# Kernel tuning notes

Hardware: AMD Instinct MI355X
Metric: run time of the kernel (lower is better)

Reference implementation:

```python
import jax, jax.numpy as jnp
import numpy as np

B, S, H = 4, 2048, 1024
NH = 16
DH = H // NH  # 64


def setup_inputs() -> dict:
    key = jax.random.key(0)
    ks = jax.random.split(key, 11)
    s = 1.0 / np.sqrt(H)
    inp = {
        "key": jax.random.normal(ks[0], (B, S, H), jnp.float32),
        "value": jax.random.normal(ks[1], (B, S, H), jnp.float32),
        "query": jax.random.normal(ks[2], (B, S, H), jnp.float32),
        # linear_layers[0] -> applied to query, [1] -> key, [2] -> value
        "wq": jax.random.normal(ks[3], (H, H), jnp.float32) * s,
        "bq": jnp.zeros((H,), jnp.float32),
        "wk": jax.random.normal(ks[4], (H, H), jnp.float32) * s,
        "bk": jnp.zeros((H,), jnp.float32),
        "wv": jax.random.normal(ks[5], (H, H), jnp.float32) * s,
        "bv": jnp.zeros((H,), jnp.float32),
        "wo": jax.random.normal(ks[6], (H, H), jnp.float32) * s,
        "bo": jnp.zeros((H,), jnp.float32),
    }
    return inp


def reference(key, value, query, wq, bq, wk, bk, wv, bv, wo, bo):
    # QKV projections; split heads -> [B, NH, S, DH]
    def proj(x, w, b):
        y = jnp.einsum("bsh,hd->bsd", x, w) + b
        return y.reshape(B, S, NH, DH).transpose(0, 2, 1, 3)

    q = proj(query, wq, bq)
    k = proj(key, wk, bk)
    v = proj(value, wv, bv)

    scores = jnp.einsum("bnqd,bnkd->bnqk", q, k) / jnp.sqrt(jnp.float32(DH))
    probs = jax.nn.softmax(scores, axis=-1)  # dropout p=0 -> identity
    out = jnp.einsum("bnqk,bnkd->bnqd", probs, v)
    out = out.transpose(0, 2, 1, 3).reshape(B, S, H)
    return jnp.einsum("bsh,hd->bsd", out, wo) + bo
```

## Files before the change

### kernel.cpp

```cpp
#include <hip/hip_runtime.h>
#include <hip/hip_bf16.h>

constexpr int kB = 4, kS = 2048, kH = 1024, kNH = 16, kDH = 64;
constexpr int kM = kB * kS;

typedef short short8 __attribute__((ext_vector_type(8)));
typedef float f32x4 __attribute__((ext_vector_type(4)));
typedef float f32x16 __attribute__((ext_vector_type(16)));

__device__ inline unsigned int pack2bf16(float lo, float hi) {
  __hip_bfloat162 h;
  h.x = __float2bfloat16(lo);
  h.y = __float2bfloat16(hi);
  unsigned int u;
  __builtin_memcpy(&u, &h, 4);
  return u;
}

__device__ inline void gload_lds16(const unsigned short* g, unsigned short* l) {
  auto* gp = (const __attribute__((address_space(1))) unsigned int*)(uintptr_t)g;
  auto* lp = (__attribute__((address_space(3))) unsigned int*)(unsigned int)(uintptr_t)l;
  __builtin_amdgcn_global_load_lds(gp, lp, 16, 0, 0);
}

__global__ __launch_bounds__(256) void f32_to_bf16_vec3(
    const float* __restrict__ i0, const float* __restrict__ i1,
    const float* __restrict__ i2, __hip_bfloat16* __restrict__ o0,
    __hip_bfloat16* __restrict__ o1, __hip_bfloat16* __restrict__ o2) {
  const int z = blockIdx.y;
  const float* in = z == 0 ? i0 : z == 1 ? i1 : i2;
  __hip_bfloat16* out = z == 0 ? o0 : z == 1 ? o1 : o2;
  const int i = blockIdx.x * 256 + threadIdx.x;
  const float4 v = ((const float4*)in)[i];
  union { __hip_bfloat16 h[4]; uint2 u; } p;
  p.h[0] = __float2bfloat16(v.x);
  p.h[1] = __float2bfloat16(v.y);
  p.h[2] = __float2bfloat16(v.z);
  p.h[3] = __float2bfloat16(v.w);
  ((uint2*)out)[i] = p.u;
}

__global__ __launch_bounds__(256) void transpose4_f32_to_bf16(
    const float* __restrict__ w0, const float* __restrict__ w1,
    const float* __restrict__ w2, const float* __restrict__ w3,
    __hip_bfloat16* __restrict__ o0, __hip_bfloat16* __restrict__ o1,
    __hip_bfloat16* __restrict__ o2, __hip_bfloat16* __restrict__ o3) {
  const int z = blockIdx.z;
  const float* in = z == 0 ? w0 : z == 1 ? w1 : z == 2 ? w2 : w3;
  __hip_bfloat16* out = z == 0 ? o0 : z == 1 ? o1 : z == 2 ? o2 : o3;
  constexpr int R = kH, C = kH;
  __shared__ float t[32][33];
  const int r0 = blockIdx.y * 32, c0 = blockIdx.x * 32;
  const int tx = threadIdx.x, ty = threadIdx.y;
#pragma unroll
  for (int i = 0; i < 32; i += 8)
    t[ty + i][tx] = in[(size_t)(r0 + ty + i) * C + c0 + tx];
  __syncthreads();
#pragma unroll
  for (int i = 0; i < 32; i += 8)
    out[(size_t)(c0 + ty + i) * R + r0 + tx] = __float2bfloat16(t[tx][ty + i]);
}

__global__ __launch_bounds__(256, 4) void gemm_qkv(
    const unsigned short* __restrict__ A0, const unsigned short* __restrict__ A1,
    const unsigned short* __restrict__ A2, const unsigned short* __restrict__ W0,
    const unsigned short* __restrict__ W1, const unsigned short* __restrict__ W2,
    const float* __restrict__ b0, const float* __restrict__ b1,
    const float* __restrict__ b2, unsigned short* __restrict__ O0,
    unsigned short* __restrict__ O1, unsigned short* __restrict__ O2) {
  constexpr int K = kH;
  __shared__ unsigned short sA[2][128 * 32];
  __shared__ unsigned short sB[2][128 * 32];
  const int tid = threadIdx.x;
  const int wave = tid >> 6, lane = tid & 63;
  const int n16 = lane & 15, quad = lane >> 4;

  const int hw = blockIdx.x + (blockIdx.y << 3) + ((int)blockIdx.z << 9);
  const int wid = (hw & 7) * 192 + (hw >> 3);
  const int z = wid >> 9;
  const int rem = wid & 511;
  const int n0 = (rem & 7) * 128, m0 = (rem >> 3) * 128;

  const unsigned short* A = z == 0 ? A0 : z == 1 ? A1 : A2;
  const unsigned short* W = z == 0 ? W0 : z == 1 ? W1 : W2;
  const float* bias = z == 0 ? b0 : z == 1 ? b1 : b2;

  const int rh = (wave >> 1) * 64, ch = (wave & 1) * 64;
  const int srow = 32 * wave + (lane >> 2);
  const int sk = (lane & 3) * 8;
  const unsigned short* gA = A + (size_t)(m0 + srow) * K + sk;
  const unsigned short* gB = W + (size_t)(n0 + srow) * K + sk;

  const f32x4 zero4 = {0.f, 0.f, 0.f, 0.f};
  f32x4 acc[4][4];
#pragma unroll
  for (int i = 0; i < 4; ++i)
#pragma unroll
    for (int j = 0; j < 4; ++j) acc[i][j] = zero4;

#pragma unroll
  for (int j = 0; j < 2; ++j) {
    gload_lds16(gA + (size_t)(16 * j) * K, &sA[0][(32 * wave + 16 * j) * 32]);
    gload_lds16(gB + (size_t)(16 * j) * K, &sB[0][(32 * wave + 16 * j) * 32]);
  }
  __syncthreads();

  int cur = 0;
  for (int k0 = 0; k0 < K; k0 += 32) {
    const int kn = (k0 + 32 < K) ? k0 + 32 : 0;
#pragma unroll
    for (int j = 0; j < 2; ++j) {
      gload_lds16(gA + (size_t)(16 * j) * K + kn,
                  &sA[cur ^ 1][(32 * wave + 16 * j) * 32]);
      gload_lds16(gB + (size_t)(16 * j) * K + kn,
                  &sB[cur ^ 1][(32 * wave + 16 * j) * 32]);
    }

    short8 af[4], bfr[4];
#pragma unroll
    for (int i = 0; i < 4; ++i)
      af[i] = *(const short8*)&sA[cur][(rh + i * 16 + n16) * 32 + quad * 8];
#pragma unroll
    for (int i = 0; i < 4; ++i)
      bfr[i] = *(const short8*)&sB[cur][(ch + i * 16 + n16) * 32 + quad * 8];
#pragma unroll
    for (int mi = 0; mi < 4; ++mi)
#pragma unroll
      for (int ni = 0; ni < 4; ++ni)
        acc[mi][ni] = __builtin_amdgcn_mfma_f32_16x16x32_bf16(
            af[mi], bfr[ni], acc[mi][ni], 0, 0, 0);

    __syncthreads();
    cur ^= 1;
  }

  __hip_bfloat16* Obf = (__hip_bfloat16*)(z == 0 ? O0 : z == 1 ? O1 : O2);
  const float osc = z == 0 ? 0.18033688011112042f : 1.0f;
#pragma unroll
  for (int ni = 0; ni < 4; ++ni) {
    const int n = n0 + ch + ni * 16 + n16;
    const float bv = bias[n];
    const int hh = n >> 6, dd = n & 63;
#pragma unroll
    for (int mi = 0; mi < 4; ++mi) {
      const int mbase = m0 + rh + mi * 16 + quad * 4;
      const int bb = mbase >> 11, ss = mbase & 2047;
      if (z == 2) {
        const size_t idx = ((size_t)(bb * kNH + hh) * kDH + dd) * kS + ss;
        uint2 w;
        w.x = pack2bf16(acc[mi][ni][0] + bv, acc[mi][ni][1] + bv);
        w.y = pack2bf16(acc[mi][ni][2] + bv, acc[mi][ni][3] + bv);
        *(uint2*)&Obf[idx] = w;
      } else {
        const size_t base = ((size_t)(bb * kNH + hh) * kS + ss) * kDH + dd;
#pragma unroll
        for (int r = 0; r < 4; ++r)
          Obf[base + (size_t)r * kDH] =
              __float2bfloat16((acc[mi][ni][r] + bv) * osc);
      }
    }
  }
}

__global__ __launch_bounds__(256) void gemm_out(
    const unsigned short* __restrict__ A, const unsigned short* __restrict__ Bt,
    const float* __restrict__ bias, float* __restrict__ C, int M, int N, int K) {
  __shared__ unsigned short sA[2][128 * 32];
  __shared__ unsigned short sB[2][128 * 32];
  const int tid = threadIdx.x;
  const int wave = tid >> 6, lane = tid & 63;
  const int n16 = lane & 15, quad = lane >> 4;

  const int hw = blockIdx.x + blockIdx.y * gridDim.x;
  const int cpx = (gridDim.x * gridDim.y) >> 3;
  const int wid = (hw & 7) * cpx + (hw >> 3);
  const int n0 = (wid % gridDim.x) * 128, m0 = (wid / gridDim.x) * 128;

  const int rh = (wave >> 1) * 64, ch = (wave & 1) * 64;
  const int srow = 32 * wave + (lane >> 2);
  const int sk = (lane & 3) * 8;
  const unsigned short* gA = A + (size_t)(m0 + srow) * K + sk;
  const unsigned short* gB = Bt + (size_t)(n0 + srow) * K + sk;

  const f32x4 zero4 = {0.f, 0.f, 0.f, 0.f};
  f32x4 acc[4][4];
#pragma unroll
  for (int i = 0; i < 4; ++i)
#pragma unroll
    for (int j = 0; j < 4; ++j) acc[i][j] = zero4;

#pragma unroll
  for (int j = 0; j < 2; ++j) {
    gload_lds16(gA + (size_t)(16 * j) * K, &sA[0][(32 * wave + 16 * j) * 32]);
    gload_lds16(gB + (size_t)(16 * j) * K, &sB[0][(32 * wave + 16 * j) * 32]);
  }
  __syncthreads();

  int cur = 0;
  for (int k0 = 0; k0 < K; k0 += 32) {
    const int kn = (k0 + 32 < K) ? k0 + 32 : 0;
#pragma unroll
    for (int j = 0; j < 2; ++j) {
      gload_lds16(gA + (size_t)(16 * j) * K + kn,
                  &sA[cur ^ 1][(32 * wave + 16 * j) * 32]);
      gload_lds16(gB + (size_t)(16 * j) * K + kn,
                  &sB[cur ^ 1][(32 * wave + 16 * j) * 32]);
    }

    short8 af[4], bfr[4];
#pragma unroll
    for (int i = 0; i < 4; ++i)
      af[i] = *(const short8*)&sA[cur][(rh + i * 16 + n16) * 32 + quad * 8];
#pragma unroll
    for (int i = 0; i < 4; ++i)
      bfr[i] = *(const short8*)&sB[cur][(ch + i * 16 + n16) * 32 + quad * 8];
#pragma unroll
    for (int mi = 0; mi < 4; ++mi)
#pragma unroll
      for (int ni = 0; ni < 4; ++ni)
        acc[mi][ni] = __builtin_amdgcn_mfma_f32_16x16x32_bf16(
            af[mi], bfr[ni], acc[mi][ni], 0, 0, 0);

    __syncthreads();
    cur ^= 1;
  }

#pragma unroll
  for (int ni = 0; ni < 4; ++ni) {
    const int n = n0 + ch + ni * 16 + n16;
    const float bv = bias[n];
#pragma unroll
    for (int mi = 0; mi < 4; ++mi) {
#pragma unroll
      for (int r = 0; r < 4; ++r) {
        const int m = m0 + rh + mi * 16 + quad * 4 + r;
        C[(size_t)m * N + n] = acc[mi][ni][r] + bv;
      }
    }
  }
}

__global__ __launch_bounds__(256, 2) void attn_mfma(
    const unsigned short* __restrict__ Q, const unsigned short* __restrict__ K,
    const unsigned short* __restrict__ V, __hip_bfloat16* __restrict__ ctx) {
  __shared__ unsigned short sK[64][72];
  __shared__ unsigned short sVT[64][72];

  const int tid = threadIdx.x;
  const int wave = tid >> 6, lane = tid & 63;
  const int l31 = lane & 31, hi = lane >> 5;

  const int hw = blockIdx.x + ((int)blockIdx.y << 3);
  const int wid = (hw & 7) * 64 + (hw >> 3);
  const int bh = wid >> 3;
  const int q0 = (wid & 7) * 256;

  const unsigned short* Qb = Q + (size_t)bh * (kS * kDH);
  const unsigned short* Kb = K + (size_t)bh * (kS * kDH);
  const unsigned short* Vb = V + (size_t)bh * (kS * kDH);

  const int qbase = q0 + wave * 64;
  short8 qf[2][4];
#pragma unroll
  for (int g = 0; g < 2; ++g)
#pragma unroll
    for (int c = 0; c < 4; ++c)
      qf[g][c] = *(const short8*)(Qb + (size_t)(qbase + g * 32 + l31) * kDH +
                                  c * 16 + hi * 8);

  float l_part0 = 0.f, l_part1 = 0.f;
  f32x16 oacc[2][2];
#pragma unroll
  for (int g = 0; g < 2; ++g)
#pragma unroll
    for (int db = 0; db < 2; ++db)
#pragma unroll
      for (int i = 0; i < 16; ++i) oacc[g][db][i] = 0.f;

  const int srow = tid >> 2, scol = (tid & 3) * 16;

  uint4 ka, kb2, va, vb;
  auto loadtile = [&](int kk) {
    ka = *(const uint4*)(Kb + (size_t)(kk + srow) * kDH + scol);
    kb2 = *(const uint4*)(Kb + (size_t)(kk + srow) * kDH + scol + 8);
    va = *(const uint4*)(Vb + (size_t)srow * kS + kk + scol);
    vb = *(const uint4*)(Vb + (size_t)srow * kS + kk + scol + 8);
  };
  auto writetile = [&]() {
    *(uint4*)&sK[srow][scol] = ka;
    *(uint4*)&sK[srow][scol + 8] = kb2;
    *(uint4*)&sVT[srow][scol] = va;
    *(uint4*)&sVT[srow][scol + 8] = vb;
  };

  loadtile(0);
  writetile();
  __syncthreads();

  for (int k0 = 0; k0 < kS; k0 += 64) {
    const int kn = (k0 + 64 < kS) ? k0 + 64 : 0;
    loadtile(kn);

    short8 pfrag[2][4];
#pragma unroll
    for (int kbi = 0; kbi < 2; ++kbi) {
      short8 af[4];
#pragma unroll
      for (int c = 0; c < 4; ++c)
        af[c] = *(const short8*)&sK[kbi * 32 + l31][c * 16 + hi * 8];
#pragma unroll
      for (int g = 0; g < 2; ++g) {
        f32x16 sacc;
#pragma unroll
        for (int i = 0; i < 16; ++i) sacc[i] = 0.f;
        __builtin_amdgcn_s_setprio(1);
#pragma unroll
        for (int c = 0; c < 4; ++c)
          sacc = __builtin_amdgcn_mfma_f32_32x32x16_bf16(af[c], qf[g][c],
                                                         sacc, 0, 0, 0);
        __builtin_amdgcn_s_setprio(0);

        unsigned int w[8];
        float lp = 0.f;
#pragma unroll
        for (int m = 0; m < 8; ++m) {
          const float p0 = __builtin_amdgcn_exp2f(sacc[2 * m]);
          const float p1 = __builtin_amdgcn_exp2f(sacc[2 * m + 1]);
          lp += p0 + p1;
          w[m] = pack2bf16(p0, p1);
        }
        if (g == 0) l_part0 += lp; else l_part1 += lp;
        asm("v_permlane32_swap_b32 %0, %1" : "+v"(w[0]), "+v"(w[2]));
        asm("v_permlane32_swap_b32 %0, %1" : "+v"(w[1]), "+v"(w[3]));
        asm("v_permlane32_swap_b32 %0, %1" : "+v"(w[4]), "+v"(w[6]));
        asm("v_permlane32_swap_b32 %0, %1" : "+v"(w[5]), "+v"(w[7]));
        union { unsigned int u[4]; short8 s; } f0, f1;
        f0.u[0] = w[0]; f0.u[1] = w[1]; f0.u[2] = w[2]; f0.u[3] = w[3];
        f1.u[0] = w[4]; f1.u[1] = w[5]; f1.u[2] = w[6]; f1.u[3] = w[7];
        pfrag[g][kbi * 2] = f0.s;
        pfrag[g][kbi * 2 + 1] = f1.s;
      }
    }

    __builtin_amdgcn_s_setprio(1);
#pragma unroll
    for (int t = 0; t < 4; ++t) {
#pragma unroll
      for (int db = 0; db < 2; ++db) {
        const short8 vf = *(const short8*)&sVT[db * 32 + l31][t * 16 + hi * 8];
        oacc[0][db] = __builtin_amdgcn_mfma_f32_32x32x16_bf16(vf, pfrag[0][t],
                                                              oacc[0][db], 0, 0, 0);
        oacc[1][db] = __builtin_amdgcn_mfma_f32_32x32x16_bf16(vf, pfrag[1][t],
                                                              oacc[1][db], 0, 0, 0);
      }
    }
    __builtin_amdgcn_s_setprio(0);

    __syncthreads();
    writetile();
    __syncthreads();
  }

  const float l0 = l_part0 + __shfl_xor(l_part0, 32);
  const float l1 = l_part1 + __shfl_xor(l_part1, 32);
  const float inv[2] = {1.f / l0, 1.f / l1};

  const int bb = bh >> 4, hh = bh & 15;
#pragma unroll
  for (int g = 0; g < 2; ++g) {
    const int qrow = qbase + g * 32 + l31;
    __hip_bfloat16* dst = ctx + ((size_t)(bb * kS + qrow)) * kH + hh * kDH;
#pragma unroll
    for (int db = 0; db < 2; ++db) {
#pragma unroll
      for (int gr = 0; gr < 4; ++gr) {
        uint2 w;
        w.x = pack2bf16(oacc[g][db][4 * gr] * inv[g],
                        oacc[g][db][4 * gr + 1] * inv[g]);
        w.y = pack2bf16(oacc[g][db][4 * gr + 2] * inv[g],
                        oacc[g][db][4 * gr + 3] * inv[g]);
        *(uint2*)(dst + db * 32 + gr * 8 + hi * 4) = w;
      }
    }
  }
}

extern "C" void kernel_launch(void* const* d_in, const int* in_sizes, int n_in,
                              void* d_out, int out_size, void* d_ws, size_t ws_size,
                              hipStream_t stream) {
  const float* key   = (const float*)d_in[0];
  const float* value = (const float*)d_in[1];
  const float* query = (const float*)d_in[2];
  const float* wq = (const float*)d_in[3];
  const float* bq = (const float*)d_in[4];
  const float* wk = (const float*)d_in[5];
  const float* bk = (const float*)d_in[6];
  const float* wv = (const float*)d_in[7];
  const float* bv = (const float*)d_in[8];
  const float* wo = (const float*)d_in[9];
  const float* bo = (const float*)d_in[10];
  float* out = (float*)d_out;

  const size_t SZ = (size_t)kB * kS * kH;
  unsigned short* p = (unsigned short*)d_ws;
  unsigned short* actb = p; p += SZ;
  unsigned short* Qh   = p; p += SZ;
  unsigned short* Kh   = p; p += SZ;
  unsigned short* Vh   = p; p += SZ;
  unsigned short* ctxh = p; p += SZ;
  unsigned short* wqt  = p; p += (size_t)kH * kH;
  unsigned short* wkt  = p; p += (size_t)kH * kH;
  unsigned short* wvt  = p; p += (size_t)kH * kH;
  unsigned short* wot  = p; p += (size_t)kH * kH;
  unsigned short* actk = ctxh;
  unsigned short* actv = (unsigned short*)out;

  const dim3 tb(32, 8);
  const dim3 tg(kH / 32, kH / 32, 4);
  transpose4_f32_to_bf16<<<tg, tb, 0, stream>>>(
      wq, wk, wv, wo, (__hip_bfloat16*)wqt, (__hip_bfloat16*)wkt,
      (__hip_bfloat16*)wvt, (__hip_bfloat16*)wot);

  const int cvblocks = (int)(SZ / 4 / 256);
  f32_to_bf16_vec3<<<dim3(cvblocks, 3), 256, 0, stream>>>(
      query, key, value, (__hip_bfloat16*)actb, (__hip_bfloat16*)actk,
      (__hip_bfloat16*)actv);

  gemm_qkv<<<dim3(kH / 128, kM / 128, 3), 256, 0, stream>>>(
      actb, actk, actv, wqt, wkt, wvt, bq, bk, bv, Qh, Kh, Vh);

  dim3 ga(kS / 256, kB * kNH);
  attn_mfma<<<ga, 256, 0, stream>>>(Qh, Kh, Vh, (__hip_bfloat16*)ctxh);

  dim3 gg(kH / 128, kM / 128);
  gemm_out<<<gg, 256, 0, stream>>>(ctxh, wot, bo, out, kM, kH, kH);
}
```

Measured before the change: 338.0 us.

## Triple-buffer GEMM K-loop and double-buffer attention K/V tiles

Replaces the double-buffered GEMM K-loop in both projection kernels with a shared triple-buffered macro. It prefetches two tiles ahead, uses explicit vmcnt waits with a single barrier per iteration, and raises MFMA priority. The attention kernel gets double-buffered K/V LDS tiles, which removes one of its two barriers per iteration. The extra LDS use lowers the GEMM occupancy hint from 4 to 3 blocks.

After: 336.3 us. Within noise of the previous version (-0.5%).

```diff
diff --git a/kernel.cpp b/kernel.cpp
--- a/kernel.cpp
+++ b/kernel.cpp
@@ -61,7 +61,53 @@
     out[(size_t)(c0 + ty + i) * R + r0 + tx] = __float2bfloat16(t[tx][ty + i]);
 }
 
-__global__ __launch_bounds__(256, 4) void gemm_qkv(
+#define GEMM_KLOOP(sA, sB, gA, gB, K, acc)                                    \
+  {                                                                           \
+    const int NIT = (K) / 32;                                                 \
+    _Pragma("unroll") for (int j = 0; j < 2; ++j) {                           \
+      gload_lds16(gA + (size_t)(16 * j) * (K), &sA[0][(32 * wave + 16 * j) * 32]); \
+      gload_lds16(gB + (size_t)(16 * j) * (K), &sB[0][(32 * wave + 16 * j) * 32]); \
+    }                                                                         \
+    _Pragma("unroll") for (int j = 0; j < 2; ++j) {                           \
+      gload_lds16(gA + (size_t)(16 * j) * (K) + 32, &sA[1][(32 * wave + 16 * j) * 32]); \
+      gload_lds16(gB + (size_t)(16 * j) * (K) + 32, &sB[1][(32 * wave + 16 * j) * 32]); \
+    }                                                                         \
+    asm volatile("s_waitcnt vmcnt(4) lgkmcnt(0)" ::: "memory");               \
+    __builtin_amdgcn_s_barrier();                                             \
+    __builtin_amdgcn_sched_barrier(0);                                        \
+    for (int t = 0; t < NIT; ++t) {                                           \
+      const int cur = t % 3;                                                  \
+      short8 af[4], bfr[4];                                                   \
+      _Pragma("unroll") for (int i = 0; i < 4; ++i)                           \
+          af[i] = *(const short8*)&sA[cur][(rh + i * 16 + n16) * 32 + quad * 8]; \
+      _Pragma("unroll") for (int i = 0; i < 4; ++i)                           \
+          bfr[i] = *(const short8*)&sB[cur][(ch + i * 16 + n16) * 32 + quad * 8]; \
+      if (t + 2 < NIT) {                                                      \
+        const int nxt = (t + 2) % 3;                                          \
+        const int kk = (t + 2) * 32;                                          \
+        _Pragma("unroll") for (int j = 0; j < 2; ++j) {                       \
+          gload_lds16(gA + (size_t)(16 * j) * (K) + kk,                       \
+                      &sA[nxt][(32 * wave + 16 * j) * 32]);                   \
+          gload_lds16(gB + (size_t)(16 * j) * (K) + kk,                       \
+                      &sB[nxt][(32 * wave + 16 * j) * 32]);                   \
+        }                                                                     \
+      }                                                                       \
+      __builtin_amdgcn_s_setprio(1);                                          \
+      _Pragma("unroll") for (int mi = 0; mi < 4; ++mi)                        \
+          _Pragma("unroll") for (int ni = 0; ni < 4; ++ni)                    \
+              acc[mi][ni] = __builtin_amdgcn_mfma_f32_16x16x32_bf16(          \
+                  af[mi], bfr[ni], acc[mi][ni], 0, 0, 0);                     \
+      __builtin_amdgcn_s_setprio(0);                                          \
+      if (t + 2 < NIT)                                                        \
+        asm volatile("s_waitcnt vmcnt(4) lgkmcnt(0)" ::: "memory");           \
+      else                                                                    \
+        asm volatile("s_waitcnt vmcnt(0) lgkmcnt(0)" ::: "memory");           \
+      __builtin_amdgcn_s_barrier();                                           \
+      __builtin_amdgcn_sched_barrier(0);                                      \
+    }                                                                         \
+  }
+
+__global__ __launch_bounds__(256, 3) void gemm_qkv(
     const unsigned short* __restrict__ A0, const unsigned short* __restrict__ A1,
     const unsigned short* __restrict__ A2, const unsigned short* __restrict__ W0,
     const unsigned short* __restrict__ W1, const unsigned short* __restrict__ W2,
@@ -69,8 +115,8 @@
     const float* __restrict__ b2, unsigned short* __restrict__ O0,
     unsigned short* __restrict__ O1, unsigned short* __restrict__ O2) {
   constexpr int K = kH;
-  __shared__ unsigned short sA[2][128 * 32];
-  __shared__ unsigned short sB[2][128 * 32];
+  __shared__ unsigned short sA[3][128 * 32];
+  __shared__ unsigned short sB[3][128 * 32];
   const int tid = threadIdx.x;
   const int wave = tid >> 6, lane = tid & 63;
   const int n16 = lane & 15, quad = lane >> 4;
@@ -98,41 +144,7 @@
 #pragma unroll
     for (int j = 0; j < 4; ++j) acc[i][j] = zero4;
 
-#pragma unroll
-  for (int j = 0; j < 2; ++j) {
-    gload_lds16(gA + (size_t)(16 * j) * K, &sA[0][(32 * wave + 16 * j) * 32]);
-    gload_lds16(gB + (size_t)(16 * j) * K, &sB[0][(32 * wave + 16 * j) * 32]);
-  }
-  __syncthreads();
-
-  int cur = 0;
-  for (int k0 = 0; k0 < K; k0 += 32) {
-    const int kn = (k0 + 32 < K) ? k0 + 32 : 0;
-#pragma unroll
-    for (int j = 0; j < 2; ++j) {
-      gload_lds16(gA + (size_t)(16 * j) * K + kn,
-                  &sA[cur ^ 1][(32 * wave + 16 * j) * 32]);
-      gload_lds16(gB + (size_t)(16 * j) * K + kn,
-                  &sB[cur ^ 1][(32 * wave + 16 * j) * 32]);
-    }
-
-    short8 af[4], bfr[4];
-#pragma unroll
-    for (int i = 0; i < 4; ++i)
-      af[i] = *(const short8*)&sA[cur][(rh + i * 16 + n16) * 32 + quad * 8];
-#pragma unroll
-    for (int i = 0; i < 4; ++i)
-      bfr[i] = *(const short8*)&sB[cur][(ch + i * 16 + n16) * 32 + quad * 8];
-#pragma unroll
-    for (int mi = 0; mi < 4; ++mi)
-#pragma unroll
-      for (int ni = 0; ni < 4; ++ni)
-        acc[mi][ni] = __builtin_amdgcn_mfma_f32_16x16x32_bf16(
-            af[mi], bfr[ni], acc[mi][ni], 0, 0, 0);
-
-    __syncthreads();
-    cur ^= 1;
-  }
+  GEMM_KLOOP(sA, sB, gA, gB, K, acc)
 
   __hip_bfloat16* Obf = (__hip_bfloat16*)(z == 0 ? O0 : z == 1 ? O1 : O2);
   const float osc = z == 0 ? 0.18033688011112042f : 1.0f;
@@ -162,11 +174,11 @@
   }
 }
 
-__global__ __launch_bounds__(256) void gemm_out(
+__global__ __launch_bounds__(256, 3) void gemm_out(
     const unsigned short* __restrict__ A, const unsigned short* __restrict__ Bt,
     const float* __restrict__ bias, float* __restrict__ C, int M, int N, int K) {
-  __shared__ unsigned short sA[2][128 * 32];
-  __shared__ unsigned short sB[2][128 * 32];
+  __shared__ unsigned short sA[3][128 * 32];
+  __shared__ unsigned short sB[3][128 * 32];
   const int tid = threadIdx.x;
   const int wave = tid >> 6, lane = tid & 63;
   const int n16 = lane & 15, quad = lane >> 4;
@@ -189,41 +201,7 @@
 #pragma unroll
     for (int j = 0; j < 4; ++j) acc[i][j] = zero4;
 
-#pragma unroll
-  for (int j = 0; j < 2; ++j) {
-    gload_lds16(gA + (size_t)(16 * j) * K, &sA[0][(32 * wave + 16 * j) * 32]);
-    gload_lds16(gB + (size_t)(16 * j) * K, &sB[0][(32 * wave + 16 * j) * 32]);
-  }
-  __syncthreads();
-
-  int cur = 0;
-  for (int k0 = 0; k0 < K; k0 += 32) {
-    const int kn = (k0 + 32 < K) ? k0 + 32 : 0;
-#pragma unroll
-    for (int j = 0; j < 2; ++j) {
-      gload_lds16(gA + (size_t)(16 * j) * K + kn,
-                  &sA[cur ^ 1][(32 * wave + 16 * j) * 32]);
-      gload_lds16(gB + (size_t)(16 * j) * K + kn,
-                  &sB[cur ^ 1][(32 * wave + 16 * j) * 32]);
-    }
-
-    short8 af[4], bfr[4];
-#pragma unroll
-    for (int i = 0; i < 4; ++i)
-      af[i] = *(const short8*)&sA[cur][(rh + i * 16 + n16) * 32 + quad * 8];
-#pragma unroll
-    for (int i = 0; i < 4; ++i)
-      bfr[i] = *(const short8*)&sB[cur][(ch + i * 16 + n16) * 32 + quad * 8];
-#pragma unroll
-    for (int mi = 0; mi < 4; ++mi)
-#pragma unroll
-      for (int ni = 0; ni < 4; ++ni)
-        acc[mi][ni] = __builtin_amdgcn_mfma_f32_16x16x32_bf16(
-            af[mi], bfr[ni], acc[mi][ni], 0, 0, 0);
-
-    __syncthreads();
-    cur ^= 1;
-  }
+  GEMM_KLOOP(sA, sB, gA, gB, K, acc)
 
 #pragma unroll
   for (int ni = 0; ni < 4; ++ni) {
@@ -243,8 +221,8 @@
 __global__ __launch_bounds__(256, 2) void attn_mfma(
     const unsigned short* __restrict__ Q, const unsigned short* __restrict__ K,
     const unsigned short* __restrict__ V, __hip_bfloat16* __restrict__ ctx) {
-  __shared__ unsigned short sK[64][72];
-  __shared__ unsigned short sVT[64][72];
+  __shared__ unsigned short sK[2][64][72];
+  __shared__ unsigned short sVT[2][64][72];
 
   const int tid = threadIdx.x;
   const int wave = tid >> 6, lane = tid & 63;
@@ -286,17 +264,18 @@
     va = *(const uint4*)(Vb + (size_t)srow * kS + kk + scol);
     vb = *(const uint4*)(Vb + (size_t)srow * kS + kk + scol + 8);
   };
-  auto writetile = [&]() {
-    *(uint4*)&sK[srow][scol] = ka;
-    *(uint4*)&sK[srow][scol + 8] = kb2;
-    *(uint4*)&sVT[srow][scol] = va;
-    *(uint4*)&sVT[srow][scol + 8] = vb;
+  auto writetile = [&](int buf) {
+    *(uint4*)&sK[buf][srow][scol] = ka;
+    *(uint4*)&sK[buf][srow][scol + 8] = kb2;
+    *(uint4*)&sVT[buf][srow][scol] = va;
+    *(uint4*)&sVT[buf][srow][scol + 8] = vb;
   };
 
   loadtile(0);
-  writetile();
+  writetile(0);
   __syncthreads();
 
+  int cur = 0;
   for (int k0 = 0; k0 < kS; k0 += 64) {
     const int kn = (k0 + 64 < kS) ? k0 + 64 : 0;
     loadtile(kn);
@@ -307,7 +286,7 @@
       short8 af[4];
 #pragma unroll
       for (int c = 0; c < 4; ++c)
-        af[c] = *(const short8*)&sK[kbi * 32 + l31][c * 16 + hi * 8];
+        af[c] = *(const short8*)&sK[cur][kbi * 32 + l31][c * 16 + hi * 8];
 #pragma unroll
       for (int g = 0; g < 2; ++g) {
         f32x16 sacc;
@@ -347,7 +326,7 @@
     for (int t = 0; t < 4; ++t) {
 #pragma unroll
       for (int db = 0; db < 2; ++db) {
-        const short8 vf = *(const short8*)&sVT[db * 32 + l31][t * 16 + hi * 8];
+        const short8 vf = *(const short8*)&sVT[cur][db * 32 + l31][t * 16 + hi * 8];
         oacc[0][db] = __builtin_amdgcn_mfma_f32_32x32x16_bf16(vf, pfrag[0][t],
                                                               oacc[0][db], 0, 0, 0);
         oacc[1][db] = __builtin_amdgcn_mfma_f32_32x32x16_bf16(vf, pfrag[1][t],
@@ -356,9 +335,9 @@
     }
     __builtin_amdgcn_s_setprio(0);
 
+    writetile(cur ^ 1);
     __syncthreads();
-    writetile();
-    __syncthreads();
+    cur ^= 1;
   }
 
   const float l0 = l_part0 + __shfl_xor(l_part0, 32);
```
